# Performance work log

Hardware: AMD Instinct MI355X
Metric: run time of the kernel (lower is better)

## Reference

```python
import jax, jax.numpy as jnp
import numpy as np

B, S, D, H = 4, 2048, 1024, 16
HD = D // H
SCALE = D ** (-0.5)  # NOTE: original scales by embedding_dim**-0.5, not head_size**-0.5


def setup_inputs() -> dict:
    key = jax.random.key(0)
    k1, k2, k3, k4, k5 = jax.random.split(key, 5)
    return {
        "x": jax.random.normal(k1, (B, S, D), dtype=jnp.float32),
        "Wqkv": jax.random.normal(k2, (3 * D, D), dtype=jnp.float32) * (D ** -0.5),
        "bqkv": jax.random.normal(k3, (3 * D,), dtype=jnp.float32) * 0.02,
        "Wlift": jax.random.normal(k4, (D, D), dtype=jnp.float32) * (D ** -0.5),
        "blift": jax.random.normal(k5, (D,), dtype=jnp.float32) * 0.02,
    }


def reference(x, Wqkv, bqkv, Wlift, blift):
    b, s, d = x.shape
    # qkv projection -> (b, s, 3, H, HD) -> (3, b, H, s, HD)
    qkv = (x @ Wqkv.T + bqkv).reshape(b, s, 3, H, HD).transpose(2, 0, 3, 1, 4)
    q, k, v = qkv[0], qkv[1], qkv[2]  # each (b, H, s, HD)
    # full score matrix, softmax over keys
    scores = jnp.einsum("bhqd,bhkd->bhqk", q, k) * SCALE
    a = jax.nn.softmax(scores, axis=-1)
    # post-hoc causal mask + renormalize (as in the original)
    a = jnp.tril(a)
    a = a / jnp.sum(a, axis=-1, keepdims=True)
    attn = jnp.einsum("bhqk,bhkd->bhqd", a, v)  # (b, H, s, HD)
    attn = attn.swapaxes(1, 2).reshape(b, s, d)  # (b, s, d)
    # lifting linear; Dropout(0.2) is identity in eval mode
    return attn @ Wlift.T + blift
```

## Files before the change

### kernel.cpp

```cpp
#include <hip/hip_runtime.h>
#include <cstdint>
#include <cstddef>

typedef unsigned short u16;
typedef unsigned int u32;
typedef __bf16 bf16x8 __attribute__((ext_vector_type(8)));
typedef float f32x4 __attribute__((ext_vector_type(4)));
typedef float f32x16 __attribute__((ext_vector_type(16)));

__device__ __forceinline__ u16 f2bf(float f) {
  unsigned u = __builtin_bit_cast(unsigned, f);
  return (u16)((u + 0x7FFFu + ((u >> 16) & 1u)) >> 16);
}

__device__ __forceinline__ u32 pk2bf(float lo, float hi) {
  union { __bf16 h[2]; u32 u; } t;
  t.h[0] = (__bf16)lo; t.h[1] = (__bf16)hi;
  return t.u;
}

__device__ __forceinline__ void gl_lds16(const void* g, void* l) {
  __builtin_amdgcn_global_load_lds(
      (const __attribute__((address_space(1))) unsigned int*)g,
      (__attribute__((address_space(3))) unsigned int*)l,
      16, 0, 0);
}

__global__ void cast4_kernel(const float* __restrict__ in, u16* __restrict__ out, int n4) {
  int i = blockIdx.x * blockDim.x + threadIdx.x;
  if (i < n4) {
    float4 v = reinterpret_cast<const float4*>(in)[i];
    ushort4 o;
    o.x = f2bf(v.x); o.y = f2bf(v.y); o.z = f2bf(v.z); o.w = f2bf(v.w);
    reinterpret_cast<ushort4*>(out)[i] = o;
  }
}

template <int EPI>
__global__ __launch_bounds__(256)
void gemm_bt_kernel(const u16* __restrict__ A, const u16* __restrict__ Bw,
                    const float* __restrict__ bias,
                    u16* __restrict__ oq, u16* __restrict__ ok, u16* __restrict__ ovT,
                    float* __restrict__ ofp, int M, int N, int K) {
  __shared__ __align__(16) u16 Als[2][128 * 32];
  __shared__ __align__(16) u16 Bls[2][128 * 32];

  const int tid = threadIdx.x;
  const int lane = tid & 63;
  const int w = tid >> 6, wr = w >> 1, wc = w & 1;
  const int lr = lane & 15, lk = lane >> 4;
  const int brow = blockIdx.y * 128, bcol = blockIdx.x * 128;

  const int srow = tid >> 2;
  const int scol = (tid & 3) << 3;
  const u16* ga = A + (size_t)(brow + srow) * K + scol;
  const u16* gb = Bw + (size_t)(bcol + srow) * K + scol;

  f32x4 acc[4][4] = {};

  auto stage = [&](int buf, int kt) {
    const u16* a0 = ga + kt * 32;
    const u16* b0 = gb + kt * 32;
    gl_lds16(a0,             &Als[buf][tid * 8]);
    gl_lds16(a0 + 64 * K,    &Als[buf][2048 + tid * 8]);
    gl_lds16(b0,             &Bls[buf][tid * 8]);
    gl_lds16(b0 + 64 * K,    &Bls[buf][2048 + tid * 8]);
  };

  stage(0, 0);
  __syncthreads();

  const int nt = K >> 5;
  int cur = 0;
  for (int t = 0; t < nt; ++t) {
    if (t + 1 < nt) stage(cur ^ 1, t + 1);
    bf16x8 af[4], bfr[4];
#pragma unroll
    for (int m = 0; m < 4; ++m)
      af[m] = *reinterpret_cast<const bf16x8*>(&Als[cur][(wr * 64 + m * 16 + lr) * 32 + lk * 8]);
#pragma unroll
    for (int n = 0; n < 4; ++n)
      bfr[n] = *reinterpret_cast<const bf16x8*>(&Bls[cur][(wc * 64 + n * 16 + lr) * 32 + lk * 8]);
#pragma unroll
    for (int m = 0; m < 4; ++m)
#pragma unroll
      for (int n = 0; n < 4; ++n)
        acc[m][n] = __builtin_amdgcn_mfma_f32_16x16x32_bf16(af[m], bfr[n], acc[m][n], 0, 0, 0);
    __syncthreads();
    cur ^= 1;
  }

  if (EPI == 0) {
    const int three = bcol >> 10;
#pragma unroll
    for (int n = 0; n < 4; ++n) {
      const int c = bcol + wc * 64 + n * 16 + lr;
      const float bv = bias[c];
      const int cc = c & 1023, h = cc >> 6, hd = cc & 63;
#pragma unroll
      for (int m = 0; m < 4; ++m) {
        const int r0 = brow + wr * 64 + m * 16 + lk * 4;
        const int b = r0 >> 11;
        const int s0 = r0 & 2047;
        if (three == 2) {
          ushort4 pkv;
          pkv.x = f2bf(acc[m][n][0] + bv);
          pkv.y = f2bf(acc[m][n][1] + bv);
          pkv.z = f2bf(acc[m][n][2] + bv);
          pkv.w = f2bf(acc[m][n][3] + bv);
          *reinterpret_cast<ushort4*>(&ovT[((size_t)(b * 16 + h) * 64 + hd) * 2048 + s0]) = pkv;
        } else {
          u16* dst = (three == 0) ? oq : ok;
          const float sc = (three == 0) ? 0.03125f * 1.44269504089f : 1.0f;
#pragma unroll
          for (int j = 0; j < 4; ++j)
            dst[((size_t)(b * 16 + h) * 2048 + (s0 + j)) * 64 + hd] = f2bf((acc[m][n][j] + bv) * sc);
        }
      }
    }
  } else {
#pragma unroll
    for (int n = 0; n < 4; ++n) {
      const int c = bcol + wc * 64 + n * 16 + lr;
      const float bv = bias[c];
#pragma unroll
      for (int m = 0; m < 4; ++m) {
        const int r0 = brow + wr * 64 + m * 16 + lk * 4;
#pragma unroll
        for (int j = 0; j < 4; ++j)
          ofp[(size_t)(r0 + j) * N + c] = acc[m][n][j] + bv;
      }
    }
  }
}

__global__ __launch_bounds__(128, 4)
void attn_causal_kernel(const u16* __restrict__ qg, const u16* __restrict__ kg_,
                        const u16* __restrict__ vT, u16* __restrict__ ob) {
  __shared__ __align__(16) u16 Kls[2][32 * 64];
  __shared__ __align__(16) u16 Vls[2][64 * 32];

  const int tid = threadIdx.x, lane = tid & 63, w = tid >> 6;
  const int n = lane & 31, hi = lane >> 5;
  const int bid = blockIdx.x;
  const int bh = bid & 63;
  const int qb = 31 - (bid >> 6);
  const int q0w = qb * 64 + w * 32;
  const int jdiag = 2 * qb + w;
  const size_t base = (size_t)bh * 2048 * 64;
  const size_t vbase = (size_t)bh * 64 * 2048;

  bf16x8 qf[4];
#pragma unroll
  for (int dc = 0; dc < 4; ++dc)
    qf[dc] = *reinterpret_cast<const bf16x8*>(
        &qg[base + (size_t)(q0w + n) * 64 + dc * 16 + hi * 8]);

  f32x16 o0 = {}, o1 = {};
  float l = 0.f;

  const int ktiles = 2 * qb + 2;

  const int lct = tid & 63;
  const int rK0 = w * 16 + (lct >> 3), cK = lct & 7;
  const int rV0 = w * 32 + (lct >> 2), cV = lct & 3;
  const u16* kgp0 = kg_ + base + (size_t)rK0 * 64 + ((cK ^ ((rK0 ^ (rK0 >> 3)) & 7)) * 8);
  const u16* kgp1 = kg_ + base + (size_t)(rK0 + 8) * 64 + ((cK ^ (((rK0 + 8) ^ ((rK0 + 8) >> 3)) & 7)) * 8);
  const u16* vgp0 = vT + vbase + (size_t)rV0 * 2048 + ((cV ^ ((rV0 ^ (rV0 >> 2)) & 3)) * 8);
  const u16* vgp1 = vT + vbase + (size_t)(rV0 + 16) * 2048 + ((cV ^ (((rV0 + 16) ^ ((rV0 + 16) >> 2)) & 3)) * 8);
  const int dK = tid * 8 + w * 512;
  const int dV = tid * 8 + w * 512;

  auto stage = [&](int buf, int t) {
    const size_t ko = (size_t)t * 2048;
    gl_lds16(kgp0 + ko, &Kls[buf][dK]);
    gl_lds16(kgp1 + ko, &Kls[buf][dK + 512]);
    gl_lds16(vgp0 + t * 32, &Vls[buf][dV]);
    gl_lds16(vgp1 + t * 32, &Vls[buf][dV + 512]);
  };

  const int swk = ((n ^ (n >> 3)) & 7) << 4;
  const int sv0 = ((n ^ (n >> 2)) & 3) << 4;
  const int sv1 = (((32 + n) ^ ((32 + n) >> 2)) & 3) << 4;

  stage(0, 0);
  __syncthreads();

  int cur = 0;
  for (int t = 0; t < ktiles; ++t) {
    if (t + 1 < ktiles) stage(cur ^ 1, t + 1);
    if (t <= jdiag) {
      const char* Kb = (const char*)&Kls[cur][0];
      const char* Vb = (const char*)&Vls[cur][0];

      f32x16 st = {};
      __builtin_amdgcn_s_setprio(1);
#pragma unroll
      for (int dc = 0; dc < 4; ++dc) {
        bf16x8 kf = *reinterpret_cast<const bf16x8*>(
            Kb + n * 128 + ((((dc << 1) | hi) << 4) ^ swk));
        st = __builtin_amdgcn_mfma_f32_32x32x16_bf16(kf, qf[dc], st, 0, 0, 0);
      }
      __builtin_amdgcn_s_setprio(0);

      if (t == jdiag) {
#pragma unroll
        for (int r = 0; r < 16; ++r) {
          const int koff = (r & 3) + 8 * (r >> 2) + 4 * hi;
          if (koff > n) st[r] = -1e30f;
        }
      }

      float rs = 0.f;
#pragma unroll
      for (int r = 0; r < 16; ++r) { st[r] = __builtin_amdgcn_exp2f(st[r]); rs += st[r]; }
      l += rs;

#pragma unroll
      for (int kk = 0; kk < 2; ++kk) {
        const int gown = (kk * 2 + hi) * 4, gsnd = (kk * 2 + (hi ^ 1)) * 4;
        u32 pa0 = pk2bf(st[gown + 0], st[gown + 1]);
        u32 pa1 = pk2bf(st[gown + 2], st[gown + 3]);
        u32 ps0 = pk2bf(st[gsnd + 0], st[gsnd + 1]);
        u32 ps1 = pk2bf(st[gsnd + 2], st[gsnd + 3]);
        u32 rA = __shfl_xor(ps0, 32, 64);
        u32 rB = __shfl_xor(ps1, 32, 64);
        union { u32 u[4]; bf16x8 v; } pb;
        pb.u[0] = hi ? rA : pa0;
        pb.u[1] = hi ? rB : pa1;
        pb.u[2] = hi ? pa0 : rA;
        pb.u[3] = hi ? pa1 : rB;
        const int c = ((kk * 2 + hi) << 4);
        __builtin_amdgcn_s_setprio(1);
        bf16x8 vf0 = *reinterpret_cast<const bf16x8*>(Vb + n * 64 + (c ^ sv0));
        o0 = __builtin_amdgcn_mfma_f32_32x32x16_bf16(vf0, pb.v, o0, 0, 0, 0);
        bf16x8 vf1 = *reinterpret_cast<const bf16x8*>(Vb + (32 + n) * 64 + (c ^ sv1));
        o1 = __builtin_amdgcn_mfma_f32_32x32x16_bf16(vf1, pb.v, o1, 0, 0, 0);
        __builtin_amdgcn_s_setprio(0);
      }
    }
    __syncthreads();
    cur ^= 1;
  }

  const int b = bh >> 4, h = bh & 15;
  const float lt = l + __shfl_xor(l, 32, 64);
  const float inv = 1.f / lt;
  const size_t rbase = ((size_t)(b * 2048 + q0w + n)) * 1024 + h * 64;
#pragma unroll
  for (int g = 0; g < 4; ++g) {
    ushort4 w0, w1;
    w0.x = f2bf(o0[g * 4 + 0] * inv); w0.y = f2bf(o0[g * 4 + 1] * inv);
    w0.z = f2bf(o0[g * 4 + 2] * inv); w0.w = f2bf(o0[g * 4 + 3] * inv);
    w1.x = f2bf(o1[g * 4 + 0] * inv); w1.y = f2bf(o1[g * 4 + 1] * inv);
    w1.z = f2bf(o1[g * 4 + 2] * inv); w1.w = f2bf(o1[g * 4 + 3] * inv);
    *reinterpret_cast<ushort4*>(&ob[rbase + g * 8 + hi * 4]) = w0;
    *reinterpret_cast<ushort4*>(&ob[rbase + 32 + g * 8 + hi * 4]) = w1;
  }
}

extern "C" void kernel_launch(void* const* d_in, const int* in_sizes, int n_in,
                              void* d_out, int out_size, void* d_ws, size_t ws_size,
                              hipStream_t stream) {
  const float* x     = (const float*)d_in[0];
  const float* Wqkv  = (const float*)d_in[1];
  const float* bqkv  = (const float*)d_in[2];
  const float* Wlift = (const float*)d_in[3];
  const float* blift = (const float*)d_in[4];
  float* out = (float*)d_out;

  if (ws_size < 40ull * 1024 * 1024) return;

  char* ws = (char*)d_ws;
  u16* xb     = (u16*)(ws);
  u16* wqkvb  = (u16*)(ws + 16777216);
  u16* wliftb = (u16*)(ws + 23068672);
  u16* vT     = (u16*)(ws + 25165824);
  u16* attnb  = xb;
  u16* qb = (u16*)d_out;
  u16* kb = qb + 8388608;

  cast4_kernel<<<8192, 256, 0, stream>>>(x, xb, 2097152);
  cast4_kernel<<<3072, 256, 0, stream>>>(Wqkv, wqkvb, 786432);
  cast4_kernel<<<1024, 256, 0, stream>>>(Wlift, wliftb, 262144);

  gemm_bt_kernel<0><<<dim3(24, 64), 256, 0, stream>>>(
      xb, wqkvb, bqkv, qb, kb, vT, nullptr, 8192, 3072, 1024);

  attn_causal_kernel<<<2048, 128, 0, stream>>>(qb, kb, vT, attnb);

  gemm_bt_kernel<1><<<dim3(8, 64), 256, 0, stream>>>(
      attnb, wliftb, blift, nullptr, nullptr, nullptr, out, 8192, 1024, 1024);
}
```

Baseline: 301.4 us.

## Enlarge attention tiles to 128 queries, triple-buffer KV, software-pipeline PV MFMAs

The attention kernel now uses 4 waves per block covering 128 query rows with 64-key tiles, cutting redundant K/V loads per query. K/V staging becomes a 3-deep ring with vmcnt-based waits instead of double buffering with __syncthreads. The P·V MFMAs of the previous slab are deferred and issued after the next QK MFMAs to overlap softmax with matrix work. This raises LDS use and register pressure and changes occupancy (launch bounds 256,3), and it adds redundant clamped prefetches at the tail.

Result: faster. 268.4 us (-10.9%).

```diff
diff --git a/kernel.cpp b/kernel.cpp
--- a/kernel.cpp
+++ b/kernel.cpp
@@ -134,19 +134,19 @@
   }
 }
 
-__global__ __launch_bounds__(128, 4)
+__global__ __launch_bounds__(256, 3)
 void attn_causal_kernel(const u16* __restrict__ qg, const u16* __restrict__ kg_,
                         const u16* __restrict__ vT, u16* __restrict__ ob) {
-  __shared__ __align__(16) u16 Kls[2][32 * 64];
-  __shared__ __align__(16) u16 Vls[2][64 * 32];
+  __shared__ __align__(16) u16 Kls[3][64 * 64];
+  __shared__ __align__(16) u16 Vls[3][64 * 64];
 
   const int tid = threadIdx.x, lane = tid & 63, w = tid >> 6;
   const int n = lane & 31, hi = lane >> 5;
   const int bid = blockIdx.x;
+  const int qbi = 15 - (bid >> 6);
   const int bh = bid & 63;
-  const int qb = 31 - (bid >> 6);
-  const int q0w = qb * 64 + w * 32;
-  const int jdiag = 2 * qb + w;
+  const int q0w = qbi * 128 + w * 32;
+  const int jdiag = qbi * 4 + w;
   const size_t base = (size_t)bh * 2048 * 64;
   const size_t vbase = (size_t)bh * 64 * 2048;
 
@@ -159,89 +159,115 @@
   f32x16 o0 = {}, o1 = {};
   float l = 0.f;
 
-  const int ktiles = 2 * qb + 2;
-
-  const int lct = tid & 63;
-  const int rK0 = w * 16 + (lct >> 3), cK = lct & 7;
-  const int rV0 = w * 32 + (lct >> 2), cV = lct & 3;
-  const u16* kgp0 = kg_ + base + (size_t)rK0 * 64 + ((cK ^ ((rK0 ^ (rK0 >> 3)) & 7)) * 8);
-  const u16* kgp1 = kg_ + base + (size_t)(rK0 + 8) * 64 + ((cK ^ (((rK0 + 8) ^ ((rK0 + 8) >> 3)) & 7)) * 8);
-  const u16* vgp0 = vT + vbase + (size_t)rV0 * 2048 + ((cV ^ ((rV0 ^ (rV0 >> 2)) & 3)) * 8);
-  const u16* vgp1 = vT + vbase + (size_t)(rV0 + 16) * 2048 + ((cV ^ (((rV0 + 16) ^ ((rV0 + 16) >> 2)) & 3)) * 8);
-  const int dK = tid * 8 + w * 512;
-  const int dV = tid * 8 + w * 512;
+  const int ktiles = qbi * 2 + 2;
+
+  const int krow = tid >> 3, kch = tid & 7;
 
   auto stage = [&](int buf, int t) {
-    const size_t ko = (size_t)t * 2048;
-    gl_lds16(kgp0 + ko, &Kls[buf][dK]);
-    gl_lds16(kgp1 + ko, &Kls[buf][dK + 512]);
-    gl_lds16(vgp0 + t * 32, &Vls[buf][dV]);
-    gl_lds16(vgp1 + t * 32, &Vls[buf][dV + 512]);
+    const int k0 = t << 6;
+#pragma unroll
+    for (int p = 0; p < 2; ++p) {
+      const int r = p * 32 + krow;
+      const int sz = (r ^ (r >> 3)) & 7;
+      gl_lds16(kg_ + base + (size_t)(k0 + r) * 64 + (kch ^ sz) * 8,
+               &Kls[buf][p * 2048 + tid * 8]);
+      gl_lds16(vT + vbase + (size_t)r * 2048 + k0 + (kch ^ sz) * 8,
+               &Vls[buf][p * 2048 + tid * 8]);
+    }
   };
 
-  const int swk = ((n ^ (n >> 3)) & 7) << 4;
-  const int sv0 = ((n ^ (n >> 2)) & 3) << 4;
-  const int sv1 = (((32 + n) ^ ((32 + n) >> 2)) & 3) << 4;
+  const int sw0 = ((n ^ (n >> 3)) & 7) << 4;
+  const int sw1 = (((32 + n) ^ ((32 + n) >> 3)) & 7) << 4;
 
   stage(0, 0);
-  __syncthreads();
-
-  int cur = 0;
+  stage(1, ktiles > 1 ? 1 : 0);
+  asm volatile("s_waitcnt vmcnt(4)" ::: "memory");
+  __builtin_amdgcn_sched_barrier(0);
+  __builtin_amdgcn_s_barrier();
+  __builtin_amdgcn_sched_barrier(0);
+
+  bf16x8 pbP0 = {}, pbP1 = {}, vfP00 = {}, vfP01 = {}, vfP10 = {}, vfP11 = {};
+  bool pend = false;
+
+  union U { u32 u[4]; bf16x8 v; };
+
+  auto slab = [&](const char* Kb, const char* Vb, int mt, bool diag) {
+    const int swK = mt ? sw1 : sw0;
+    f32x16 st = {};
+    __builtin_amdgcn_s_setprio(1);
+#pragma unroll
+    for (int dc = 0; dc < 4; ++dc) {
+      bf16x8 kf = *reinterpret_cast<const bf16x8*>(
+          Kb + (mt * 32 + n) * 128 + ((((dc << 1) | hi) << 4) ^ swK));
+      st = __builtin_amdgcn_mfma_f32_32x32x16_bf16(kf, qf[dc], st, 0, 0, 0);
+    }
+    if (pend) {
+      o0 = __builtin_amdgcn_mfma_f32_32x32x16_bf16(vfP00, pbP0, o0, 0, 0, 0);
+      o1 = __builtin_amdgcn_mfma_f32_32x32x16_bf16(vfP01, pbP0, o1, 0, 0, 0);
+      o0 = __builtin_amdgcn_mfma_f32_32x32x16_bf16(vfP10, pbP1, o0, 0, 0, 0);
+      o1 = __builtin_amdgcn_mfma_f32_32x32x16_bf16(vfP11, pbP1, o1, 0, 0, 0);
+    }
+    __builtin_amdgcn_s_setprio(0);
+    if (diag) {
+#pragma unroll
+      for (int r = 0; r < 16; ++r) {
+        const int koff = (r & 3) + 8 * (r >> 2) + 4 * hi;
+        if (koff > n) st[r] = -1e30f;
+      }
+    }
+    float rs = 0.f;
+#pragma unroll
+    for (int r = 0; r < 16; ++r) { st[r] = __builtin_amdgcn_exp2f(st[r]); rs += st[r]; }
+    l += rs;
+#pragma unroll
+    for (int kk = 0; kk < 2; ++kk) {
+      const int gown = (kk * 2 + hi) * 4, gsnd = (kk * 2 + (hi ^ 1)) * 4;
+      u32 pa0 = pk2bf(st[gown + 0], st[gown + 1]);
+      u32 pa1 = pk2bf(st[gown + 2], st[gown + 3]);
+      u32 ps0 = pk2bf(st[gsnd + 0], st[gsnd + 1]);
+      u32 ps1 = pk2bf(st[gsnd + 2], st[gsnd + 3]);
+      u32 rA = __shfl_xor(ps0, 32, 64);
+      u32 rB = __shfl_xor(ps1, 32, 64);
+      U pb;
+      pb.u[0] = hi ? rA : pa0;
+      pb.u[1] = hi ? rB : pa1;
+      pb.u[2] = hi ? pa0 : rA;
+      pb.u[3] = hi ? pa1 : rB;
+      if (kk == 0) pbP0 = pb.v; else pbP1 = pb.v;
+    }
+    const int c0 = ((mt * 4 + hi) << 4);
+    const int c1 = ((mt * 4 + 2 + hi) << 4);
+    vfP00 = *reinterpret_cast<const bf16x8*>(Vb + n * 128 + (c0 ^ sw0));
+    vfP01 = *reinterpret_cast<const bf16x8*>(Vb + (32 + n) * 128 + (c0 ^ sw1));
+    vfP10 = *reinterpret_cast<const bf16x8*>(Vb + n * 128 + (c1 ^ sw0));
+    vfP11 = *reinterpret_cast<const bf16x8*>(Vb + (32 + n) * 128 + (c1 ^ sw1));
+    pend = true;
+  };
+
   for (int t = 0; t < ktiles; ++t) {
-    if (t + 1 < ktiles) stage(cur ^ 1, t + 1);
-    if (t <= jdiag) {
-      const char* Kb = (const char*)&Kls[cur][0];
-      const char* Vb = (const char*)&Vls[cur][0];
-
-      f32x16 st = {};
-      __builtin_amdgcn_s_setprio(1);
-#pragma unroll
-      for (int dc = 0; dc < 4; ++dc) {
-        bf16x8 kf = *reinterpret_cast<const bf16x8*>(
-            Kb + n * 128 + ((((dc << 1) | hi) << 4) ^ swk));
-        st = __builtin_amdgcn_mfma_f32_32x32x16_bf16(kf, qf[dc], st, 0, 0, 0);
-      }
-      __builtin_amdgcn_s_setprio(0);
-
-      if (t == jdiag) {
-#pragma unroll
-        for (int r = 0; r < 16; ++r) {
-          const int koff = (r & 3) + 8 * (r >> 2) + 4 * hi;
-          if (koff > n) st[r] = -1e30f;
-        }
-      }
-
-      float rs = 0.f;
-#pragma unroll
-      for (int r = 0; r < 16; ++r) { st[r] = __builtin_amdgcn_exp2f(st[r]); rs += st[r]; }
-      l += rs;
-
-#pragma unroll
-      for (int kk = 0; kk < 2; ++kk) {
-        const int gown = (kk * 2 + hi) * 4, gsnd = (kk * 2 + (hi ^ 1)) * 4;
-        u32 pa0 = pk2bf(st[gown + 0], st[gown + 1]);
-        u32 pa1 = pk2bf(st[gown + 2], st[gown + 3]);
-        u32 ps0 = pk2bf(st[gsnd + 0], st[gsnd + 1]);
-        u32 ps1 = pk2bf(st[gsnd + 2], st[gsnd + 3]);
-        u32 rA = __shfl_xor(ps0, 32, 64);
-        u32 rB = __shfl_xor(ps1, 32, 64);
-        union { u32 u[4]; bf16x8 v; } pb;
-        pb.u[0] = hi ? rA : pa0;
-        pb.u[1] = hi ? rB : pa1;
-        pb.u[2] = hi ? pa0 : rA;
-        pb.u[3] = hi ? pa1 : rB;
-        const int c = ((kk * 2 + hi) << 4);
-        __builtin_amdgcn_s_setprio(1);
-        bf16x8 vf0 = *reinterpret_cast<const bf16x8*>(Vb + n * 64 + (c ^ sv0));
-        o0 = __builtin_amdgcn_mfma_f32_32x32x16_bf16(vf0, pb.v, o0, 0, 0, 0);
-        bf16x8 vf1 = *reinterpret_cast<const bf16x8*>(Vb + (32 + n) * 64 + (c ^ sv1));
-        o1 = __builtin_amdgcn_mfma_f32_32x32x16_bf16(vf1, pb.v, o1, 0, 0, 0);
-        __builtin_amdgcn_s_setprio(0);
-      }
-    }
-    __syncthreads();
-    cur ^= 1;
-  }
+    const int tpre = (t + 2 < ktiles) ? (t + 2) : (ktiles - 1);
+    stage((t + 2) % 3, tpre);
+    const char* Kb = (const char*)&Kls[t % 3][0];
+    const char* Vb = (const char*)&Vls[t % 3][0];
+    const int e0 = 2 * t;
+    if (e0 <= jdiag) slab(Kb, Vb, 0, e0 == jdiag);
+    if (e0 + 1 <= jdiag) slab(Kb, Vb, 1, e0 + 1 == jdiag);
+    asm volatile("s_waitcnt vmcnt(4)" ::: "memory");
+    __builtin_amdgcn_sched_barrier(0);
+    __builtin_amdgcn_s_barrier();
+    __builtin_amdgcn_sched_barrier(0);
+  }
+
+  if (pend) {
+    __builtin_amdgcn_s_setprio(1);
+    o0 = __builtin_amdgcn_mfma_f32_32x32x16_bf16(vfP00, pbP0, o0, 0, 0, 0);
+    o1 = __builtin_amdgcn_mfma_f32_32x32x16_bf16(vfP01, pbP0, o1, 0, 0, 0);
+    o0 = __builtin_amdgcn_mfma_f32_32x32x16_bf16(vfP10, pbP1, o0, 0, 0, 0);
+    o1 = __builtin_amdgcn_mfma_f32_32x32x16_bf16(vfP11, pbP1, o1, 0, 0, 0);
+    __builtin_amdgcn_s_setprio(0);
+  }
+
+  asm volatile("s_waitcnt vmcnt(0)" ::: "memory");
 
   const int b = bh >> 4, h = bh & 15;
   const float lt = l + __shfl_xor(l, 32, 64);
@@ -287,7 +313,7 @@
   gemm_bt_kernel<0><<<dim3(24, 64), 256, 0, stream>>>(
       xb, wqkvb, bqkv, qb, kb, vT, nullptr, 8192, 3072, 1024);
 
-  attn_causal_kernel<<<2048, 128, 0, stream>>>(qb, kb, vT, attnb);
+  attn_causal_kernel<<<1024, 256, 0, stream>>>(qb, kb, vT, attnb);
 
   gemm_bt_kernel<1><<<dim3(8, 64), 256, 0, stream>>>(
       attnb, wliftb, blift, nullptr, nullptr, nullptr, out, 8192, 1024, 1024);
```

## Give each attention wave private K/V LDS buffers and drop block barriers

Applied to the files above, without the earlier changes.

Restructures the causal attention kernel so each of four waves in a 256-thread block owns its own double-buffered K/V LDS tiles. Each wave loads and iterates only its own causal range, synchronising with waitcnt instead of __syncthreads. The QK^T MFMA chain is split into two independent accumulators to shorten the dependency chain. Waves no longer stall on each other or run idle iterations, at the cost of more LDS per block and no K/V reuse across waves.

Measured after the change: 302.4 us. About the same (+0.3%).

```diff
diff --git a/kernel.cpp b/kernel.cpp
--- a/kernel.cpp
+++ b/kernel.cpp
@@ -134,19 +134,19 @@
   }
 }
 
-__global__ __launch_bounds__(128, 4)
+__global__ __launch_bounds__(256, 2)
 void attn_causal_kernel(const u16* __restrict__ qg, const u16* __restrict__ kg_,
                         const u16* __restrict__ vT, u16* __restrict__ ob) {
-  __shared__ __align__(16) u16 Kls[2][32 * 64];
-  __shared__ __align__(16) u16 Vls[2][64 * 32];
+  __shared__ __align__(16) u16 Kls[4][2][32 * 64];
+  __shared__ __align__(16) u16 Vls[4][2][64 * 32];
 
   const int tid = threadIdx.x, lane = tid & 63, w = tid >> 6;
   const int n = lane & 31, hi = lane >> 5;
   const int bid = blockIdx.x;
+  const int qbi = 15 - (bid >> 6);
   const int bh = bid & 63;
-  const int qb = 31 - (bid >> 6);
-  const int q0w = qb * 64 + w * 32;
-  const int jdiag = 2 * qb + w;
+  const int j = qbi * 4 + w;
+  const int q0w = j * 32;
   const size_t base = (size_t)bh * 2048 * 64;
   const size_t vbase = (size_t)bh * 64 * 2048;
 
@@ -159,24 +159,24 @@
   f32x16 o0 = {}, o1 = {};
   float l = 0.f;
 
-  const int ktiles = 2 * qb + 2;
-
-  const int lct = tid & 63;
-  const int rK0 = w * 16 + (lct >> 3), cK = lct & 7;
-  const int rV0 = w * 32 + (lct >> 2), cV = lct & 3;
-  const u16* kgp0 = kg_ + base + (size_t)rK0 * 64 + ((cK ^ ((rK0 ^ (rK0 >> 3)) & 7)) * 8);
-  const u16* kgp1 = kg_ + base + (size_t)(rK0 + 8) * 64 + ((cK ^ (((rK0 + 8) ^ ((rK0 + 8) >> 3)) & 7)) * 8);
-  const u16* vgp0 = vT + vbase + (size_t)rV0 * 2048 + ((cV ^ ((rV0 ^ (rV0 >> 2)) & 3)) * 8);
-  const u16* vgp1 = vT + vbase + (size_t)(rV0 + 16) * 2048 + ((cV ^ (((rV0 + 16) ^ ((rV0 + 16) >> 2)) & 3)) * 8);
-  const int dK = tid * 8 + w * 512;
-  const int dV = tid * 8 + w * 512;
+  const int l3 = lane >> 3, cK = lane & 7;
+  const int l2 = lane >> 2, cV = lane & 3;
+  const int svz = (l2 & 3) ^ (l2 >> 2);
+  int ko[4], vo[4];
+#pragma unroll
+  for (int p = 0; p < 4; ++p) {
+    ko[p] = (p * 8 + l3) * 64 + ((cK ^ l3 ^ p) & 7) * 8;
+    vo[p] = (p * 16 + l2) * 2048 + ((cV ^ svz) & 3) * 8;
+  }
+  u16* kd = &Kls[w][0][lane * 8];
+  u16* vd = &Vls[w][0][lane * 8];
 
   auto stage = [&](int buf, int t) {
-    const size_t ko = (size_t)t * 2048;
-    gl_lds16(kgp0 + ko, &Kls[buf][dK]);
-    gl_lds16(kgp1 + ko, &Kls[buf][dK + 512]);
-    gl_lds16(vgp0 + t * 32, &Vls[buf][dV]);
-    gl_lds16(vgp1 + t * 32, &Vls[buf][dV + 512]);
+#pragma unroll
+    for (int p = 0; p < 4; ++p) {
+      gl_lds16(kg_ + base + (size_t)t * 2048 + ko[p], kd + buf * 2048 + p * 512);
+      gl_lds16(vT + vbase + vo[p] + t * 32,           vd + buf * 2048 + p * 512);
+    }
   };
 
   const int swk = ((n ^ (n >> 3)) & 7) << 4;
@@ -184,64 +184,71 @@
   const int sv1 = (((32 + n) ^ ((32 + n) >> 2)) & 3) << 4;
 
   stage(0, 0);
-  __syncthreads();
-
-  int cur = 0;
-  for (int t = 0; t < ktiles; ++t) {
-    if (t + 1 < ktiles) stage(cur ^ 1, t + 1);
-    if (t <= jdiag) {
-      const char* Kb = (const char*)&Kls[cur][0];
-      const char* Vb = (const char*)&Vls[cur][0];
-
-      f32x16 st = {};
+
+  for (int t = 0; t <= j; ++t) {
+    asm volatile("s_waitcnt lgkmcnt(0)" ::: "memory");
+    const int tn = (t + 1 <= j) ? (t + 1) : j;
+    stage((t + 1) & 1, tn);
+    asm volatile("s_waitcnt vmcnt(8)" ::: "memory");
+    __builtin_amdgcn_sched_barrier(0);
+
+    const char* Kb = (const char*)&Kls[w][t & 1][0];
+    const char* Vb = (const char*)&Vls[w][t & 1][0];
+
+    bf16x8 kf0 = *reinterpret_cast<const bf16x8*>(Kb + n * 128 + ((0 * 32 + hi * 16) ^ swk));
+    bf16x8 kf1 = *reinterpret_cast<const bf16x8*>(Kb + n * 128 + ((1 * 32 + hi * 16) ^ swk));
+    bf16x8 kf2 = *reinterpret_cast<const bf16x8*>(Kb + n * 128 + ((2 * 32 + hi * 16) ^ swk));
+    bf16x8 kf3 = *reinterpret_cast<const bf16x8*>(Kb + n * 128 + ((3 * 32 + hi * 16) ^ swk));
+    f32x16 stE = {}, stF = {};
+    __builtin_amdgcn_s_setprio(1);
+    stE = __builtin_amdgcn_mfma_f32_32x32x16_bf16(kf0, qf[0], stE, 0, 0, 0);
+    stF = __builtin_amdgcn_mfma_f32_32x32x16_bf16(kf1, qf[1], stF, 0, 0, 0);
+    stE = __builtin_amdgcn_mfma_f32_32x32x16_bf16(kf2, qf[2], stE, 0, 0, 0);
+    stF = __builtin_amdgcn_mfma_f32_32x32x16_bf16(kf3, qf[3], stF, 0, 0, 0);
+    __builtin_amdgcn_s_setprio(0);
+
+    f32x16 st;
+#pragma unroll
+    for (int r = 0; r < 16; ++r) st[r] = stE[r] + stF[r];
+
+    if (t == j) {
+#pragma unroll
+      for (int r = 0; r < 16; ++r) {
+        const int koff = (r & 3) + 8 * (r >> 2) + 4 * hi;
+        if (koff > n) st[r] = -1e30f;
+      }
+    }
+
+    float rs = 0.f;
+#pragma unroll
+    for (int r = 0; r < 16; ++r) { st[r] = __builtin_amdgcn_exp2f(st[r]); rs += st[r]; }
+    l += rs;
+
+#pragma unroll
+    for (int kk = 0; kk < 2; ++kk) {
+      const int gown = (kk * 2 + hi) * 4, gsnd = (kk * 2 + (hi ^ 1)) * 4;
+      u32 pa0 = pk2bf(st[gown + 0], st[gown + 1]);
+      u32 pa1 = pk2bf(st[gown + 2], st[gown + 3]);
+      u32 ps0 = pk2bf(st[gsnd + 0], st[gsnd + 1]);
+      u32 ps1 = pk2bf(st[gsnd + 2], st[gsnd + 3]);
+      u32 rA = __shfl_xor(ps0, 32, 64);
+      u32 rB = __shfl_xor(ps1, 32, 64);
+      union { u32 u[4]; bf16x8 v; } pb;
+      pb.u[0] = hi ? rA : pa0;
+      pb.u[1] = hi ? rB : pa1;
+      pb.u[2] = hi ? pa0 : rA;
+      pb.u[3] = hi ? pa1 : rB;
+      const int c = ((kk * 2 + hi) << 4);
+      bf16x8 vf0 = *reinterpret_cast<const bf16x8*>(Vb + n * 64 + (c ^ sv0));
+      bf16x8 vf1 = *reinterpret_cast<const bf16x8*>(Vb + (32 + n) * 64 + (c ^ sv1));
       __builtin_amdgcn_s_setprio(1);
-#pragma unroll
-      for (int dc = 0; dc < 4; ++dc) {
-        bf16x8 kf = *reinterpret_cast<const bf16x8*>(
-            Kb + n * 128 + ((((dc << 1) | hi) << 4) ^ swk));
-        st = __builtin_amdgcn_mfma_f32_32x32x16_bf16(kf, qf[dc], st, 0, 0, 0);
-      }
+      o0 = __builtin_amdgcn_mfma_f32_32x32x16_bf16(vf0, pb.v, o0, 0, 0, 0);
+      o1 = __builtin_amdgcn_mfma_f32_32x32x16_bf16(vf1, pb.v, o1, 0, 0, 0);
       __builtin_amdgcn_s_setprio(0);
-
-      if (t == jdiag) {
-#pragma unroll
-        for (int r = 0; r < 16; ++r) {
-          const int koff = (r & 3) + 8 * (r >> 2) + 4 * hi;
-          if (koff > n) st[r] = -1e30f;
-        }
-      }
-
-      float rs = 0.f;
-#pragma unroll
-      for (int r = 0; r < 16; ++r) { st[r] = __builtin_amdgcn_exp2f(st[r]); rs += st[r]; }
-      l += rs;
-
-#pragma unroll
-      for (int kk = 0; kk < 2; ++kk) {
-        const int gown = (kk * 2 + hi) * 4, gsnd = (kk * 2 + (hi ^ 1)) * 4;
-        u32 pa0 = pk2bf(st[gown + 0], st[gown + 1]);
-        u32 pa1 = pk2bf(st[gown + 2], st[gown + 3]);
-        u32 ps0 = pk2bf(st[gsnd + 0], st[gsnd + 1]);
-        u32 ps1 = pk2bf(st[gsnd + 2], st[gsnd + 3]);
-        u32 rA = __shfl_xor(ps0, 32, 64);
-        u32 rB = __shfl_xor(ps1, 32, 64);
-        union { u32 u[4]; bf16x8 v; } pb;
-        pb.u[0] = hi ? rA : pa0;
-        pb.u[1] = hi ? rB : pa1;
-        pb.u[2] = hi ? pa0 : rA;
-        pb.u[3] = hi ? pa1 : rB;
-        const int c = ((kk * 2 + hi) << 4);
-        __builtin_amdgcn_s_setprio(1);
-        bf16x8 vf0 = *reinterpret_cast<const bf16x8*>(Vb + n * 64 + (c ^ sv0));
-        o0 = __builtin_amdgcn_mfma_f32_32x32x16_bf16(vf0, pb.v, o0, 0, 0, 0);
-        bf16x8 vf1 = *reinterpret_cast<const bf16x8*>(Vb + (32 + n) * 64 + (c ^ sv1));
-        o1 = __builtin_amdgcn_mfma_f32_32x32x16_bf16(vf1, pb.v, o1, 0, 0, 0);
-        __builtin_amdgcn_s_setprio(0);
-      }
-    }
-    __syncthreads();
-    cur ^= 1;
-  }
+    }
+  }
+
+  asm volatile("s_waitcnt vmcnt(0)" ::: "memory");
 
   const int b = bh >> 4, h = bh & 15;
   const float lt = l + __shfl_xor(l, 32, 64);
@@ -287,7 +294,7 @@
   gemm_bt_kernel<0><<<dim3(24, 64), 256, 0, stream>>>(
       xb, wqkvb, bqkv, qb, kb, vT, nullptr, 8192, 3072, 1024);
 
-  attn_causal_kernel<<<2048, 128, 0, stream>>>(qb, kb, vT, attnb);
+  attn_causal_kernel<<<1024, 256, 0, stream>>>(qb, kb, vT, attnb);
 
   gemm_bt_kernel<1><<<dim3(8, 64), 256, 0, stream>>>(
       attnb, wliftb, blift, nullptr, nullptr, nullptr, out, 8192, 1024, 1024);
```
